# Optimization experiments

Hardware: AMD Instinct MI355X
Metric: run time of the kernel (lower is better)

Reference implementation:

```python
import jax, jax.numpy as jnp
import numpy as np

B, H, W, C = 16, 64, 64, 512
WS, SS, NH = 8, 4, 16
HD = C // NH
N = WS * WS          # tokens per window = 64
NWH, NWW = H // WS, W // WS
NW = NWH * NWW       # windows per image = 64
HID = 2048
EPS = 1e-5

def _rel_pos_index():
    coords = np.stack(np.meshgrid(np.arange(WS), np.arange(WS), indexing='ij'))  # [2,ws,ws]
    cf = coords.reshape(2, -1)                      # [2,N]
    rel = cf[:, :, None] - cf[:, None, :]           # [2,N,N]
    rel = rel.transpose(1, 2, 0).astype(np.int64)   # [N,N,2]
    rel[:, :, 0] += WS - 1
    rel[:, :, 1] += WS - 1
    rel[:, :, 0] *= 2 * WS - 1
    return rel.sum(-1)                              # [N,N]

def _attn_mask():
    img = np.zeros((H, W), dtype=np.float32)
    cnt = 0
    sls = (slice(0, -WS), slice(-WS, -SS), slice(-SS, None))
    for hs in sls:
        for ws_ in sls:
            img[hs, ws_] = cnt
            cnt += 1
    mw = img.reshape(NWH, WS, NWW, WS).transpose(0, 2, 1, 3).reshape(-1, N)  # [nW,N]
    am = mw[:, None, :] - mw[:, :, None]            # [nW,N,N] (unsqueeze(1)-unsqueeze(2))
    return np.where(am != 0, np.float32(-100.0), np.float32(0.0))

_RPI = jnp.asarray(_rel_pos_index())
_AMASK = jnp.asarray(_attn_mask())

def _ln(x, g, b):
    m = jnp.mean(x, -1, keepdims=True)
    v = jnp.mean((x - m) ** 2, -1, keepdims=True)
    return (x - m) * jax.lax.rsqrt(v + EPS) * g + b

def setup_inputs() -> dict:
    key = jax.random.key(0)
    ks = jax.random.split(key, 8)
    s = 0.02
    return {
        'x': jax.random.normal(ks[0], (B, H * W, C), jnp.float32),
        'g1': jnp.ones((C,), jnp.float32), 'b1': jnp.zeros((C,), jnp.float32),
        'qkv_w': jax.random.normal(ks[1], (C, 3 * C), jnp.float32) * s,
        'qkv_b': jnp.zeros((3 * C,), jnp.float32),
        'proj_w': jax.random.normal(ks[2], (C, C), jnp.float32) * s,
        'proj_b': jnp.zeros((C,), jnp.float32),
        'rpb': jax.random.normal(ks[3], ((2 * WS - 1) ** 2, NH), jnp.float32) * s,
        'g2': jnp.ones((C,), jnp.float32), 'b2': jnp.zeros((C,), jnp.float32),
        'fc1_w': jax.random.normal(ks[4], (C, HID), jnp.float32) * s,
        'fc1_b': jnp.zeros((HID,), jnp.float32),
        'fc2_w': jax.random.normal(ks[5], (HID, C), jnp.float32) * s,
        'fc2_b': jnp.zeros((C,), jnp.float32),
    }

def reference(x, g1, b1, qkv_w, qkv_b, proj_w, proj_b, rpb, g2, b2, fc1_w, fc1_b, fc2_w, fc2_b):
    shortcut = x                                    # [B,L,C]
    xn = _ln(x, g1, b1).reshape(B, H, W, C)
    xs = jnp.roll(xn, (-SS, -SS), axis=(1, 2))      # cyclic shift
    # window partition -> [B*nW, N, C]
    xw = xs.reshape(B, NWH, WS, NWW, WS, C).transpose(0, 1, 3, 2, 4, 5).reshape(-1, N, C)
    # attention
    qkv = xw @ qkv_w + qkv_b                        # [Bw,N,3C]
    qkv = qkv.reshape(-1, N, 3, NH, HD).transpose(2, 0, 3, 1, 4)  # [3,Bw,NH,N,HD]
    q, k, v = qkv[0], qkv[1], qkv[2]
    scale = jnp.asarray(HD ** -0.5, xw.dtype)
    attn = jnp.einsum('bhnd,bhmd->bhnm', q, k) * scale            # [Bw,NH,N,N]
    bias = rpb[_RPI.reshape(-1)].reshape(N, N, NH).transpose(2, 0, 1)
    attn = attn + bias[None]
    attn = attn.reshape(B, NW, NH, N, N) + _AMASK[None, :, None]
    attn = jax.nn.softmax(attn.reshape(-1, NH, N, N), axis=-1)
    out = jnp.einsum('bhnm,bhmd->bhnd', attn, v)    # [Bw,NH,N,HD]
    out = out.transpose(0, 2, 1, 3).reshape(-1, N, C)
    out = out @ proj_w + proj_b
    # window reverse -> [B,H,W,C]
    xr = out.reshape(B, NWH, NWW, WS, WS, C).transpose(0, 1, 3, 2, 4, 5).reshape(B, H, W, C)
    xr = jnp.roll(xr, (SS, SS), axis=(1, 2)).reshape(B, H * W, C)
    x = shortcut + xr
    h = _ln(x, g2, b2)
    h = jax.nn.gelu(h @ fc1_w + fc1_b, approximate=False) @ fc2_w + fc2_b
    return x + h
```

## Files before the change

### kernel.cpp

```cpp
#include <hip/hip_runtime.h>
#include <hip/hip_bf16.h>

using f32x4  = __attribute__((ext_vector_type(4))) float;
using bf16x8 = __attribute__((ext_vector_type(8))) short;
using short8 = __attribute__((ext_vector_type(8))) short;
using s16x4  = __attribute__((ext_vector_type(4))) short;

#define DEVINL __device__ __forceinline__

DEVINL short f2bf(float f) {
  unsigned u = __builtin_bit_cast(unsigned, f);
  u += 0x7fffu + ((u >> 16) & 1u);
  return (short)(u >> 16);
}

DEVINL float gelu_tanh(float v) {
  float c = v * (0.79788456080286536f + 0.0356774081363001f * v * v);
  return 0.5f * v * (1.0f + tanhf(c));
}

#define GLDS16(g, l) __builtin_amdgcn_global_load_lds( \
    (const __attribute__((address_space(1))) void*)(g), \
    (__attribute__((address_space(3))) void*)(l), 16, 0, 0)

#define SBAR() __builtin_amdgcn_s_barrier()
#define WAITV(n) asm volatile("s_waitcnt vmcnt(" #n ")" ::: "memory")
#define WAITL0() do { asm volatile("s_waitcnt lgkmcnt(0)" ::: "memory"); \
                      __builtin_amdgcn_sched_barrier(0); } while (0)

__global__ __launch_bounds__(256)
void transpose_bf16(const float* __restrict__ in, short* __restrict__ out, int R, int C) {
  int idx = blockIdx.x * 256 + threadIdx.x;
  if (idx >= R * C) return;
  int c = idx / R, r = idx % R;
  out[idx] = f2bf(in[(size_t)r * C + c]);
}

__global__ __launch_bounds__(256)
void bias_expand(const float* __restrict__ rpb, float* __restrict__ BIASF) {
  int idx = blockIdx.x * 256 + threadIdx.x;
  int head = idx >> 12, n = (idx >> 6) & 63, m = idx & 63;
  int i1 = n >> 3, j1 = n & 7, i2 = m >> 3, j2 = m & 7;
  BIASF[idx] = rpb[((i1 - i2 + 7) * 15 + (j1 - j2 + 7)) * 16 + head];
}

template<int REMAP>
__global__ __launch_bounds__(256)
void ln_kernel(const float* __restrict__ X, const float* __restrict__ gamma,
               const float* __restrict__ beta, short* __restrict__ OUT) {
  const int lane = threadIdx.x & 63;
  const int wid  = threadIdx.x >> 6;
  const int t    = blockIdx.x * 4 + wid;
  const float* xp = X + (size_t)t * 512 + lane * 8;
  float4 a = *(const float4*)xp;
  float4 b = *(const float4*)(xp + 4);
  float s = a.x + a.y + a.z + a.w + b.x + b.y + b.z + b.w;
  float q = a.x*a.x + a.y*a.y + a.z*a.z + a.w*a.w
          + b.x*b.x + b.y*b.y + b.z*b.z + b.w*b.w;
#pragma unroll
  for (int d = 1; d < 64; d <<= 1) { s += __shfl_xor(s, d); q += __shfl_xor(q, d); }
  float mean = s * (1.0f / 512.0f);
  float var  = q * (1.0f / 512.0f) - mean * mean;
  float rstd = rsqrtf(var + 1e-5f);
  float4 g0 = *(const float4*)(gamma + lane * 8);
  float4 g1 = *(const float4*)(gamma + lane * 8 + 4);
  float4 b0 = *(const float4*)(beta + lane * 8);
  float4 b1 = *(const float4*)(beta + lane * 8 + 4);
  short8 o;
  o[0] = f2bf((a.x - mean) * rstd * g0.x + b0.x);
  o[1] = f2bf((a.y - mean) * rstd * g0.y + b0.y);
  o[2] = f2bf((a.z - mean) * rstd * g0.z + b0.z);
  o[3] = f2bf((a.w - mean) * rstd * g0.w + b0.w);
  o[4] = f2bf((b.x - mean) * rstd * g1.x + b1.x);
  o[5] = f2bf((b.y - mean) * rstd * g1.y + b1.y);
  o[6] = f2bf((b.z - mean) * rstd * g1.z + b1.z);
  o[7] = f2bf((b.w - mean) * rstd * g1.w + b1.w);
  size_t orow;
  if (REMAP) {
    int bb = t >> 12, l = t & 4095, hh = l >> 6, ww = l & 63;
    int hs = (hh + 60) & 63, ws2 = (ww + 60) & 63;
    orow = (size_t)(bb * 64 + (hs >> 3) * 8 + (ws2 >> 3)) * 64 + (hs & 7) * 8 + (ws2 & 7);
  } else {
    orow = (size_t)t;
  }
  *(short8*)(OUT + orow * 512 + lane * 8) = o;
}

__global__ __launch_bounds__(256)
void attn_core(const short* __restrict__ Q, const short* __restrict__ Kb,
               const short* __restrict__ VT, const float* __restrict__ BIASF,
               short* __restrict__ AOUT) {
  __shared__ short P[4][4096];
  const int tid = threadIdx.x, lane = tid & 63, wid = tid >> 6;
  const int lr = lane & 15, lg = lane >> 4;
  const int gw = blockIdx.x * 4 + wid;
  const int win = gw >> 4, head = gw & 15;
  const int wimg = win & 63, wh = wimg >> 3, ww = wimg & 7;
  const size_t qbase = (size_t)win * 64 * 512 + head * 32;
  short* Pb = P[wid];

  bf16x8 aq[4], bk[4];
#pragma unroll
  for (int tm = 0; tm < 4; ++tm) aq[tm] = *(const bf16x8*)(Q  + qbase + (size_t)(tm * 16 + lr) * 512 + lg * 8);
#pragma unroll
  for (int tn = 0; tn < 4; ++tn) bk[tn] = *(const bf16x8*)(Kb + qbase + (size_t)(tn * 16 + lr) * 512 + lg * 8);
  f32x4 sa[4][4] = {};
#pragma unroll
  for (int tm = 0; tm < 4; ++tm)
#pragma unroll
    for (int tn = 0; tn < 4; ++tn)
      sa[tm][tn] = __builtin_amdgcn_mfma_f32_16x16x32_bf16(aq[tm], bk[tn], sa[tm][tn], 0, 0, 0);

  const float* bias_h = BIASF + head * 4096;
  float inv[4][4];
#pragma unroll
  for (int tm = 0; tm < 4; ++tm) {
#pragma unroll
    for (int e = 0; e < 4; ++e) {
      const int n = tm * 16 + lg * 4 + e;
      const int i1 = n >> 3, j1 = n & 7;
      const int rh1 = (wh == 7) ? 1 + (i1 >> 2) : 0;
      const int rw1 = (ww == 7) ? 1 + (j1 >> 2) : 0;
      float v[4];
      float mx = -3.0e38f;
#pragma unroll
      for (int tn = 0; tn < 4; ++tn) {
        const int m = tn * 16 + lr;
        const int mi = (m >> 3), mj = m & 7;
        const int rh2 = (wh == 7) ? 1 + (mi >> 2) : 0;
        const int rw2 = (ww == 7) ? 1 + (mj >> 2) : 0;
        float val = sa[tm][tn][e] + bias_h[n * 64 + m]
                  + ((rh1 != rh2 || rw1 != rw2) ? -100.0f : 0.0f);
        v[tn] = val;
        mx = fmaxf(mx, val);
      }
#pragma unroll
      for (int d = 1; d < 16; d <<= 1) mx = fmaxf(mx, __shfl_xor(mx, d));
      float sum = 0.f;
#pragma unroll
      for (int tn = 0; tn < 4; ++tn) { v[tn] = __expf(v[tn] - mx); sum += v[tn]; }
#pragma unroll
      for (int d = 1; d < 16; d <<= 1) sum += __shfl_xor(sum, d);
      inv[tm][e] = 1.0f / sum;
      const int sw = (n & 7) << 3;
#pragma unroll
      for (int tn = 0; tn < 4; ++tn) Pb[n * 64 + ((tn * 16 + lr) ^ sw)] = f2bf(v[tn]);
    }
  }
  __syncthreads();

  f32x4 oa[4][2] = {};
  const short* vt = VT + (size_t)win * 32768 + head * 2048;
#pragma unroll
  for (int ks = 0; ks < 2; ++ks) {
    bf16x8 pa[4], bv[2];
#pragma unroll
    for (int tm = 0; tm < 4; ++tm) {
      const int r = tm * 16 + lr;
      pa[tm] = *(const bf16x8*)(Pb + r * 64 + ((ks * 32 + lg * 8) ^ ((r & 7) << 3)));
    }
#pragma unroll
    for (int t2 = 0; t2 < 2; ++t2) bv[t2] = *(const bf16x8*)(vt + (t2 * 16 + lr) * 64 + ks * 32 + lg * 8);
#pragma unroll
    for (int tm = 0; tm < 4; ++tm)
#pragma unroll
      for (int t2 = 0; t2 < 2; ++t2)
        oa[tm][t2] = __builtin_amdgcn_mfma_f32_16x16x32_bf16(pa[tm], bv[t2], oa[tm][t2], 0, 0, 0);
  }
#pragma unroll
  for (int tm = 0; tm < 4; ++tm)
#pragma unroll
    for (int t2 = 0; t2 < 2; ++t2)
#pragma unroll
      for (int e = 0; e < 4; ++e) {
        const int n = tm * 16 + lg * 4 + e;
        AOUT[((size_t)win * 64 + n) * 512 + head * 32 + t2 * 16 + lr] = f2bf(oa[tm][t2][e] * inv[tm][e]);
      }
}

template<int EPI, int K>
__global__ __launch_bounds__(512, 1)
void gemm256(const short* __restrict__ Aa, const short* __restrict__ Bb,
             const float* __restrict__ bias, const float* __restrict__ resid,
             float* __restrict__ outf, short* __restrict__ outh) {
  constexpr int NT = K / 32;
  __shared__ short L[3][2][2][128 * 32];
  const int tid = threadIdx.x;
  const int lane = tid & 63, w = tid >> 6;
  const int lr = lane & 15, lg = lane >> 4;
  const int wm = w >> 2, wn = w & 3;

  const int nwg = gridDim.x;
  const int id = blockIdx.x;
  const int id2 = (id & 7) * (nwg >> 3) + (id >> 3);
  int mt, ntile;
  if (EPI == 1) { mt = id2 & 7; ntile = id2 >> 3; }
  else          { ntile = id2 & 1; mt = id2 >> 1; }
  const int m0 = mt * 256, n0 = ntile * 256;

  const int srow = w * 16 + (lane >> 2);
  const int pcb  = (lane & 3) * 16;
  const int scol = ((lane & 3) * 8) ^ (((srow >> 1) & 3) * 8);

  auto stage = [&](int slot, int mat, int half, int kt) {
    const short* src = mat ? Bb : Aa;
    const int rbase = (mat ? n0 : m0) + half * 128;
    GLDS16(src + (size_t)(rbase + srow) * K + kt * 32 + scol,
           (short*)&L[slot][mat][half][0] + srow * 32 + (pcb >> 1));
  };
  auto lda = [&](int slot, int mr) -> bf16x8 {
    const int row = mr * 16 + lr;
    const int cb = (lg * 16) ^ (((row >> 1) & 3) * 16);
    return *(const bf16x8*)((const char*)&L[slot][0][wm][0] + row * 64 + cb);
  };
  auto ldb = [&](int slot, int nr) -> bf16x8 {
    const int row = (wn & 1) * 64 + nr * 16 + lr;
    const int cb = (lg * 16) ^ (((row >> 1) & 3) * 16);
    return *(const bf16x8*)((const char*)&L[slot][1][wn >> 1][0] + row * 64 + cb);
  };

  f32x4 acc[8][4] = {};
#pragma unroll
  for (int u = 0; u < 2; ++u) {
    stage(u, 0, 0, u); stage(u, 0, 1, u);
    stage(u, 1, 0, u); stage(u, 1, 1, u);
  }
  WAITV(4);
  SBAR();

  bf16x8 b[4];
  for (int t = 0; t < NT; ++t) {
    const int slot = t % 3;
    const int s2 = (t + 2) % 3;
    bf16x8 a0[4];
#pragma unroll
    for (int i = 0; i < 4; ++i) a0[i] = lda(slot, i);
#pragma unroll
    for (int j = 0; j < 4; ++j) b[j] = ldb(slot, j);
    if (t + 2 < NT) { stage(s2, 0, 0, t + 2); stage(s2, 0, 1, t + 2); }
    SBAR();
    WAITL0();
    __builtin_amdgcn_s_setprio(1);
#pragma unroll
    for (int i = 0; i < 4; ++i)
#pragma unroll
      for (int j = 0; j < 4; ++j)
        acc[i][j] = __builtin_amdgcn_mfma_f32_16x16x32_bf16(a0[i], b[j], acc[i][j], 0, 0, 0);
    __builtin_amdgcn_s_setprio(0);
    SBAR();
    bf16x8 a1[4];
#pragma unroll
    for (int i = 0; i < 4; ++i) a1[i] = lda(slot, 4 + i);
    if (t + 2 < NT) { stage(s2, 1, 0, t + 2); stage(s2, 1, 1, t + 2); }
    SBAR();
    WAITL0();
    __builtin_amdgcn_s_setprio(1);
#pragma unroll
    for (int i = 0; i < 4; ++i)
#pragma unroll
      for (int j = 0; j < 4; ++j)
        acc[4 + i][j] = __builtin_amdgcn_mfma_f32_16x16x32_bf16(a1[i], b[j], acc[4 + i][j], 0, 0, 0);
    __builtin_amdgcn_s_setprio(0);
    if (t < NT - 2)       { WAITV(4); }
    else if (t == NT - 2) { WAITV(0); }
    SBAR();
  }

  if (EPI == 1) {
#pragma unroll
    for (int mr = 0; mr < 8; ++mr) {
      const int h0 = m0 + wm * 128 + mr * 16 + lg * 4;
      const float4 bi = *(const float4*)(bias + h0);
#pragma unroll
      for (int nr = 0; nr < 4; ++nr) {
        const int tok = n0 + wn * 64 + nr * 16 + lr;
        s16x4 o;
        o[0] = f2bf(gelu_tanh(acc[mr][nr][0] + bi.x));
        o[1] = f2bf(gelu_tanh(acc[mr][nr][1] + bi.y));
        o[2] = f2bf(gelu_tanh(acc[mr][nr][2] + bi.z));
        o[3] = f2bf(gelu_tanh(acc[mr][nr][3] + bi.w));
        *(s16x4*)(outh + (size_t)tok * 2048 + h0) = o;
      }
    }
  } else {
#pragma unroll
    for (int nr = 0; nr < 4; ++nr) {
      const int col = n0 + wn * 64 + nr * 16 + lr;
      const float bc = bias[col];
#pragma unroll
      for (int mr = 0; mr < 8; ++mr)
#pragma unroll
        for (int e = 0; e < 4; ++e) {
          const int row = m0 + wm * 128 + mr * 16 + lg * 4 + e;
          outf[(size_t)row * 512 + col] = acc[mr][nr][e] + bc + resid[(size_t)row * 512 + col];
        }
    }
  }
}

template<int EPI>
__global__ __launch_bounds__(256, 2)
void gemm128(const short* __restrict__ A, const short* __restrict__ BT,
             const int N, const int K,
             const float* __restrict__ bias,
             const float* __restrict__ resid,
             float* __restrict__ outf, short* __restrict__ outh) {
  __shared__ short As[128 * 32];
  __shared__ short Bs[128 * 32];
  const int tid = threadIdx.x, lane = tid & 63, wid = tid >> 6;
  const int lr = lane & 15, lg = lane >> 4;
  const int wm = wid >> 1, wn = wid & 1;
  const int m0 = blockIdx.y * 128, n0 = blockIdx.x * 128;
  const int srow = lane >> 2;
  const int scol = (lane & 3) * 8;
  f32x4 acc[4][4] = {};
  for (int kt = 0; kt < K; kt += 32) {
#pragma unroll
    for (int c = 0; c < 2; ++c) {
      const int chunk = wid * 2 + c;
      GLDS16(A  + (size_t)(m0 + chunk * 16 + srow) * K + kt + scol, As + chunk * 512);
      GLDS16(BT + (size_t)(n0 + chunk * 16 + srow) * K + kt + scol, Bs + chunk * 512);
    }
    __syncthreads();
    bf16x8 af[4], bf_[4];
#pragma unroll
    for (int t = 0; t < 4; ++t) af[t]  = *(const bf16x8*)(As + (wm * 64 + t * 16 + lr) * 32 + lg * 8);
#pragma unroll
    for (int t = 0; t < 4; ++t) bf_[t] = *(const bf16x8*)(Bs + (wn * 64 + t * 16 + lr) * 32 + lg * 8);
#pragma unroll
    for (int i = 0; i < 4; ++i)
#pragma unroll
      for (int j = 0; j < 4; ++j)
        acc[i][j] = __builtin_amdgcn_mfma_f32_16x16x32_bf16(af[i], bf_[j], acc[i][j], 0, 0, 0);
    __syncthreads();
  }
#pragma unroll
  for (int j = 0; j < 4; ++j) {
    const int col = n0 + wn * 64 + j * 16 + lr;
    const float bc = bias[col];
#pragma unroll
    for (int i = 0; i < 4; ++i)
#pragma unroll
      for (int e = 0; e < 4; ++e) {
        const int row = m0 + wm * 64 + i * 16 + lg * 4 + e;
        float v = acc[i][j][e] + bc;
        if (EPI == 0) {
          const int w = row >> 6, n = row & 63;
          const int bb = w >> 6, wi = w & 63;
          const int hs = (wi >> 3) * 8 + (n >> 3), ws2 = (wi & 7) * 8 + (n & 7);
          const int hh = (hs + 4) & 63, wwp = (ws2 + 4) & 63;
          const size_t orow = (size_t)bb * 4096 + hh * 64 + wwp;
          outf[orow * 512 + col] = resid[orow * 512 + col] + v;
        } else {
          const int seg = col >> 9;
          if (seg == 0) {
            outh[(size_t)row * 512 + col] = f2bf(v * 0.17677669529663687f);
          } else if (seg == 1) {
            outh[33554432 + (size_t)row * 512 + (col - 512)] = f2bf(v);
          } else {
            const int cc = col - 1024;
            outh[67108864 + (size_t)((row >> 6) * 16 + (cc >> 5)) * 2048 + (cc & 31) * 64 + (row & 63)] = f2bf(v);
          }
        }
      }
  }
}

extern "C" void kernel_launch(void* const* d_in, const int* in_sizes, int n_in,
                              void* d_out, int out_size, void* d_ws, size_t ws_size,
                              hipStream_t stream) {
  (void)in_sizes; (void)n_in; (void)out_size; (void)ws_size;
  const float* x      = (const float*)d_in[0];
  const float* g1     = (const float*)d_in[1];
  const float* b1     = (const float*)d_in[2];
  const float* qkv_w  = (const float*)d_in[3];
  const float* qkv_b  = (const float*)d_in[4];
  const float* proj_w = (const float*)d_in[5];
  const float* proj_b = (const float*)d_in[6];
  const float* rpb    = (const float*)d_in[7];
  const float* g2     = (const float*)d_in[8];
  const float* b2     = (const float*)d_in[9];
  const float* fc1_w  = (const float*)d_in[10];
  const float* fc1_b  = (const float*)d_in[11];
  const float* fc2_w  = (const float*)d_in[12];
  const float* fc2_b  = (const float*)d_in[13];
  float* out = (float*)d_out;
  char* ws = (char*)d_ws;

  short* WQKVT  = (short*)(ws);
  short* WPROJT = (short*)(ws + 1572864);
  short* WFC1T  = (short*)(ws + 2097152);
  short* WFC2T  = (short*)(ws + 4194304);
  float* X2     = (float*)(ws + 6291456);
  float* BIASF  = (float*)(ws + 6291456);
  short* ATT    = (short*)(ws + 140509184);
  short* XW     = (short*)(ws + 207618048);
  short* QB     = (short*)(ws + 274726912);
  short* H1     = XW;
  short* X2N    = ATT;

  transpose_bf16<<<3072, 256, 0, stream>>>(qkv_w,  WQKVT, 512, 1536);
  transpose_bf16<<<1024, 256, 0, stream>>>(proj_w, WPROJT, 512, 512);
  transpose_bf16<<<4096, 256, 0, stream>>>(fc1_w,  WFC1T, 512, 2048);
  transpose_bf16<<<4096, 256, 0, stream>>>(fc2_w,  WFC2T, 2048, 512);
  bias_expand<<<256, 256, 0, stream>>>(rpb, BIASF);

  ln_kernel<1><<<16384, 256, 0, stream>>>(x, g1, b1, XW);
  gemm128<3><<<dim3(12, 512), 256, 0, stream>>>(XW, WQKVT, 1536, 512, qkv_b, nullptr, nullptr, QB);
  attn_core<<<4096, 256, 0, stream>>>(QB, QB + 33554432, QB + 67108864, BIASF, ATT);
  gemm128<0><<<dim3(4, 512), 256, 0, stream>>>(ATT, WPROJT, 512, 512, proj_b, x, X2, nullptr);
  ln_kernel<0><<<16384, 256, 0, stream>>>(X2, g2, b2, X2N);
  gemm256<1, 512><<<2048, 512, 0, stream>>>(WFC1T, X2N, fc1_b, nullptr, nullptr, H1);
  gemm256<2, 2048><<<512, 512, 0, stream>>>(H1, WFC2T, fc2_b, X2, out, nullptr);
}
```

Before: 992.1 us.

## Simplify gemm256 main loop, route proj GEMM to gemm256, faster GELU

The gemm256 main loop now issues all four staging loads at once and computes all 8x4 MFMAs per k-step with fewer barriers and lgkm waits, using precomputed LDS offsets. The output projection moves from the 128-tile GEMM to the 256-tile kernel through a new EPI==0 epilogue that does the window-reverse, roll and residual add. GELU uses an exp plus reciprocal sigmoid form instead of tanhf. Fewer barriers reduce sync overhead but also remove the split that let LDS reads overlap with MFMAs, and the extra live fragments raise register pressure.

```diff
diff --git a/kernel.cpp b/kernel.cpp
--- a/kernel.cpp
+++ b/kernel.cpp
@@ -14,9 +14,9 @@
   return (short)(u >> 16);
 }
 
-DEVINL float gelu_tanh(float v) {
-  float c = v * (0.79788456080286536f + 0.0356774081363001f * v * v);
-  return 0.5f * v * (1.0f + tanhf(c));
+DEVINL float gelu_fast(float v) {
+  float t = __expf(-1.5957691216057308f * (v + 0.044715f * v * v * v));
+  return v * __builtin_amdgcn_rcpf(1.0f + t);
 }
 
 #define GLDS16(g, l) __builtin_amdgcn_global_load_lds( \
@@ -25,8 +25,6 @@
 
 #define SBAR() __builtin_amdgcn_s_barrier()
 #define WAITV(n) asm volatile("s_waitcnt vmcnt(" #n ")" ::: "memory")
-#define WAITL0() do { asm volatile("s_waitcnt lgkmcnt(0)" ::: "memory"); \
-                      __builtin_amdgcn_sched_barrier(0); } while (0)
 
 __global__ __launch_bounds__(256)
 void transpose_bf16(const float* __restrict__ in, short* __restrict__ out, int R, int C) {
@@ -201,65 +199,53 @@
   const int srow = w * 16 + (lane >> 2);
   const int pcb  = (lane & 3) * 16;
   const int scol = ((lane & 3) * 8) ^ (((srow >> 1) & 3) * 8);
-
-  auto stage = [&](int slot, int mat, int half, int kt) {
-    const short* src = mat ? Bb : Aa;
-    const int rbase = (mat ? n0 : m0) + half * 128;
-    GLDS16(src + (size_t)(rbase + srow) * K + kt * 32 + scol,
-           (short*)&L[slot][mat][half][0] + srow * 32 + (pcb >> 1));
+  const short* gA0 = Aa + (size_t)(m0 +       srow) * K + scol;
+  const short* gA1 = Aa + (size_t)(m0 + 128 + srow) * K + scol;
+  const short* gB0 = Bb + (size_t)(n0 +       srow) * K + scol;
+  const short* gB1 = Bb + (size_t)(n0 + 128 + srow) * K + scol;
+  const int dOff = srow * 64 + pcb;
+  char* Lb = (char*)&L[0][0][0][0];
+
+  auto stageAll = [&](int slot, int kt) {
+    char* s = Lb + slot * 32768 + dOff;
+    GLDS16(gA0 + kt * 32, s);
+    GLDS16(gA1 + kt * 32, s + 8192);
+    GLDS16(gB0 + kt * 32, s + 16384);
+    GLDS16(gB1 + kt * 32, s + 24576);
   };
-  auto lda = [&](int slot, int mr) -> bf16x8 {
+
+  int aoff[8], boff[4];
+#pragma unroll
+  for (int mr = 0; mr < 8; ++mr) {
     const int row = mr * 16 + lr;
-    const int cb = (lg * 16) ^ (((row >> 1) & 3) * 16);
-    return *(const bf16x8*)((const char*)&L[slot][0][wm][0] + row * 64 + cb);
-  };
-  auto ldb = [&](int slot, int nr) -> bf16x8 {
+    aoff[mr] = wm * 8192 + row * 64 + ((lg * 16) ^ (((row >> 1) & 3) * 16));
+  }
+#pragma unroll
+  for (int nr = 0; nr < 4; ++nr) {
     const int row = (wn & 1) * 64 + nr * 16 + lr;
-    const int cb = (lg * 16) ^ (((row >> 1) & 3) * 16);
-    return *(const bf16x8*)((const char*)&L[slot][1][wn >> 1][0] + row * 64 + cb);
-  };
+    boff[nr] = 16384 + (wn >> 1) * 8192 + row * 64 + ((lg * 16) ^ (((row >> 1) & 3) * 16));
+  }
 
   f32x4 acc[8][4] = {};
-#pragma unroll
-  for (int u = 0; u < 2; ++u) {
-    stage(u, 0, 0, u); stage(u, 0, 1, u);
-    stage(u, 1, 0, u); stage(u, 1, 1, u);
-  }
+  stageAll(0, 0);
+  stageAll(1, 1);
   WAITV(4);
   SBAR();
 
-  bf16x8 b[4];
   for (int t = 0; t < NT; ++t) {
-    const int slot = t % 3;
-    const int s2 = (t + 2) % 3;
-    bf16x8 a0[4];
-#pragma unroll
-    for (int i = 0; i < 4; ++i) a0[i] = lda(slot, i);
-#pragma unroll
-    for (int j = 0; j < 4; ++j) b[j] = ldb(slot, j);
-    if (t + 2 < NT) { stage(s2, 0, 0, t + 2); stage(s2, 0, 1, t + 2); }
-    SBAR();
-    WAITL0();
+    const char* Ls = Lb + (t % 3) * 32768;
+    bf16x8 a[8], b[4];
+#pragma unroll
+    for (int i = 0; i < 8; ++i) a[i] = *(const bf16x8*)(Ls + aoff[i]);
+#pragma unroll
+    for (int j = 0; j < 4; ++j) b[j] = *(const bf16x8*)(Ls + boff[j]);
+    if (t + 2 < NT) stageAll((t + 2) % 3, t + 2);
     __builtin_amdgcn_s_setprio(1);
 #pragma unroll
-    for (int i = 0; i < 4; ++i)
+    for (int i = 0; i < 8; ++i)
 #pragma unroll
       for (int j = 0; j < 4; ++j)
-        acc[i][j] = __builtin_amdgcn_mfma_f32_16x16x32_bf16(a0[i], b[j], acc[i][j], 0, 0, 0);
-    __builtin_amdgcn_s_setprio(0);
-    SBAR();
-    bf16x8 a1[4];
-#pragma unroll
-    for (int i = 0; i < 4; ++i) a1[i] = lda(slot, 4 + i);
-    if (t + 2 < NT) { stage(s2, 1, 0, t + 2); stage(s2, 1, 1, t + 2); }
-    SBAR();
-    WAITL0();
-    __builtin_amdgcn_s_setprio(1);
-#pragma unroll
-    for (int i = 0; i < 4; ++i)
-#pragma unroll
-      for (int j = 0; j < 4; ++j)
-        acc[4 + i][j] = __builtin_amdgcn_mfma_f32_16x16x32_bf16(a1[i], b[j], acc[4 + i][j], 0, 0, 0);
+        acc[i][j] = __builtin_amdgcn_mfma_f32_16x16x32_bf16(a[i], b[j], acc[i][j], 0, 0, 0);
     __builtin_amdgcn_s_setprio(0);
     if (t < NT - 2)       { WAITV(4); }
     else if (t == NT - 2) { WAITV(0); }
@@ -275,12 +261,31 @@
       for (int nr = 0; nr < 4; ++nr) {
         const int tok = n0 + wn * 64 + nr * 16 + lr;
         s16x4 o;
-        o[0] = f2bf(gelu_tanh(acc[mr][nr][0] + bi.x));
-        o[1] = f2bf(gelu_tanh(acc[mr][nr][1] + bi.y));
-        o[2] = f2bf(gelu_tanh(acc[mr][nr][2] + bi.z));
-        o[3] = f2bf(gelu_tanh(acc[mr][nr][3] + bi.w));
+        o[0] = f2bf(gelu_fast(acc[mr][nr][0] + bi.x));
+        o[1] = f2bf(gelu_fast(acc[mr][nr][1] + bi.y));
+        o[2] = f2bf(gelu_fast(acc[mr][nr][2] + bi.z));
+        o[3] = f2bf(gelu_fast(acc[mr][nr][3] + bi.w));
         *(s16x4*)(outh + (size_t)tok * 2048 + h0) = o;
       }
+    }
+  } else if (EPI == 0) {
+#pragma unroll
+    for (int nr = 0; nr < 4; ++nr) {
+      const int col = n0 + wn * 64 + nr * 16 + lr;
+      const float bc = bias[col];
+#pragma unroll
+      for (int mr = 0; mr < 8; ++mr)
+#pragma unroll
+        for (int e = 0; e < 4; ++e) {
+          const int row = m0 + wm * 128 + mr * 16 + lg * 4 + e;
+          float v = acc[mr][nr][e] + bc;
+          const int wv = row >> 6, n = row & 63;
+          const int bb = wv >> 6, wi = wv & 63;
+          const int hs = (wi >> 3) * 8 + (n >> 3), ws2 = (wi & 7) * 8 + (n & 7);
+          const int hh = (hs + 4) & 63, wwp = (ws2 + 4) & 63;
+          const size_t orow = (size_t)bb * 4096 + hh * 64 + wwp;
+          outf[orow * 512 + col] = resid[orow * 512 + col] + v;
+        }
     }
   } else {
 #pragma unroll
@@ -298,13 +303,10 @@
   }
 }
 
-template<int EPI>
 __global__ __launch_bounds__(256, 2)
-void gemm128(const short* __restrict__ A, const short* __restrict__ BT,
-             const int N, const int K,
-             const float* __restrict__ bias,
-             const float* __restrict__ resid,
-             float* __restrict__ outf, short* __restrict__ outh) {
+void gemm128_qkv(const short* __restrict__ A, const short* __restrict__ BT,
+                 const float* __restrict__ bias, short* __restrict__ outh) {
+  constexpr int K = 512;
   __shared__ short As[128 * 32];
   __shared__ short Bs[128 * 32];
   const int tid = threadIdx.x, lane = tid & 63, wid = tid >> 6;
@@ -344,23 +346,14 @@
       for (int e = 0; e < 4; ++e) {
         const int row = m0 + wm * 64 + i * 16 + lg * 4 + e;
         float v = acc[i][j][e] + bc;
-        if (EPI == 0) {
-          const int w = row >> 6, n = row & 63;
-          const int bb = w >> 6, wi = w & 63;
-          const int hs = (wi >> 3) * 8 + (n >> 3), ws2 = (wi & 7) * 8 + (n & 7);
-          const int hh = (hs + 4) & 63, wwp = (ws2 + 4) & 63;
-          const size_t orow = (size_t)bb * 4096 + hh * 64 + wwp;
-          outf[orow * 512 + col] = resid[orow * 512 + col] + v;
+        const int seg = col >> 9;
+        if (seg == 0) {
+          outh[(size_t)row * 512 + col] = f2bf(v * 0.17677669529663687f);
+        } else if (seg == 1) {
+          outh[33554432 + (size_t)row * 512 + (col - 512)] = f2bf(v);
         } else {
-          const int seg = col >> 9;
-          if (seg == 0) {
-            outh[(size_t)row * 512 + col] = f2bf(v * 0.17677669529663687f);
-          } else if (seg == 1) {
-            outh[33554432 + (size_t)row * 512 + (col - 512)] = f2bf(v);
-          } else {
-            const int cc = col - 1024;
-            outh[67108864 + (size_t)((row >> 6) * 16 + (cc >> 5)) * 2048 + (cc & 31) * 64 + (row & 63)] = f2bf(v);
-          }
+          const int cc = col - 1024;
+          outh[67108864 + (size_t)((row >> 6) * 16 + (cc >> 5)) * 2048 + (cc & 31) * 64 + (row & 63)] = f2bf(v);
         }
       }
   }
@@ -406,9 +399,9 @@
   bias_expand<<<256, 256, 0, stream>>>(rpb, BIASF);
 
   ln_kernel<1><<<16384, 256, 0, stream>>>(x, g1, b1, XW);
-  gemm128<3><<<dim3(12, 512), 256, 0, stream>>>(XW, WQKVT, 1536, 512, qkv_b, nullptr, nullptr, QB);
+  gemm128_qkv<<<dim3(12, 512), 256, 0, stream>>>(XW, WQKVT, qkv_b, QB);
   attn_core<<<4096, 256, 0, stream>>>(QB, QB + 33554432, QB + 67108864, BIASF, ATT);
-  gemm128<0><<<dim3(4, 512), 256, 0, stream>>>(ATT, WPROJT, 512, 512, proj_b, x, X2, nullptr);
+  gemm256<0, 512><<<512, 512, 0, stream>>>(ATT, WPROJT, proj_b, x, X2, nullptr);
   ln_kernel<0><<<16384, 256, 0, stream>>>(X2, g2, b2, X2N);
   gemm256<1, 512><<<2048, 512, 0, stream>>>(WFC1T, X2N, fc1_b, nullptr, nullptr, H1);
   gemm256<2, 2048><<<512, 512, 0, stream>>>(H1, WFC2T, fc2_b, X2, out, nullptr);
```

Result: faster. 873.8 us (-11.9%).
